# Optimization experiments

Hardware: AMD Instinct MI355X
Metric: run time of the kernel (lower is better)

## Reference

```python
import jax, jax.numpy as jnp
from jax import lax
import numpy as np

EPS = 1e-5
ALPHA = 0.2  # LeakyReLU slope


def setup_inputs() -> dict:
    key = jax.random.key(0)
    ks = jax.random.split(key, 8)
    B, N, F_IN, HID, OUT, H = 32, 512, 256, 512, 512, 4
    D = OUT // H
    return {
        "x": jax.random.normal(ks[0], (B, N, F_IN), dtype=jnp.float32),
        "adj": jax.random.uniform(ks[1], (N, N), dtype=jnp.float32),
        "gc_w": jax.random.normal(ks[2], (F_IN, HID), dtype=jnp.float32) * 0.04,
        "gc_b": jax.random.normal(ks[3], (HID,), dtype=jnp.float32) * 0.04,
        "bn1_g": jnp.ones((HID,), jnp.float32),
        "bn1_b": jnp.zeros((HID,), jnp.float32),
        "bn1_m": jnp.zeros((HID,), jnp.float32),
        "bn1_v": jnp.ones((HID,), jnp.float32),
        "gat_w": jax.random.normal(ks[4], (H, D, HID), dtype=jnp.float32) * 0.04,
        "conv_w": jax.random.normal(ks[5], (OUT, OUT, 3), dtype=jnp.float32) * 0.02,
        "conv_b": jax.random.normal(ks[6], (OUT,), dtype=jnp.float32) * 0.02,
        "bn2_g": jnp.ones((OUT,), jnp.float32),
        "bn2_b": jnp.zeros((OUT,), jnp.float32),
        "bn2_m": jnp.zeros((OUT,), jnp.float32),
        "bn2_v": jnp.ones((OUT,), jnp.float32),
    }


def reference(x, adj, gc_w, gc_b, bn1_g, bn1_b, bn1_m, bn1_v, gat_w,
              conv_w, conv_b, bn2_g, bn2_b, bn2_m, bn2_v):
    # --- GraphConvolution: adj @ (x @ W) + b ---
    support = jnp.einsum('bnc,cd->bnd', x, gc_w)
    g = jnp.einsum('nm,bmd->bnd', adj, support) + gc_b  # [B,N,HID]
    # --- BatchNorm1d over channel dim (eval mode) + ReLU ---
    g = (g - bn1_m) * (bn1_g / jnp.sqrt(bn1_v + EPS)) + bn1_b
    g = jax.nn.relu(g)
    # --- Multi-head GAT (repeat/mul/sum == attention-weighted matmul) ---
    hh = jnp.einsum('bnf,hdf->bhnd', g, gat_w)           # per-head projections
    e = jnp.einsum('bhnd,bhmd->bhnm', hh, hh)            # logits [B,H,N,N]
    e = jnp.where(e > 0, e, ALPHA * e)                   # LeakyReLU
    att = jax.nn.softmax(e, axis=-1)
    o = jnp.einsum('bhnm,bhmd->bhnd', att, hh)
    B, H, N, D = o.shape
    o = o.transpose(0, 2, 1, 3).reshape(B, N, H * D)     # concat heads [B,N,OUT]
    # --- TCN block: conv1d(k=3,pad=1) over node axis + BN(eval) + ReLU ---
    xc = o.transpose(0, 2, 1)                            # [B,C,N]
    y = lax.conv_general_dilated(xc, conv_w, (1,), ((1, 1),),
                                 dimension_numbers=('NCH', 'OIH', 'NCH'))
    y = y + conv_b[None, :, None]
    y = (y - bn2_m[None, :, None]) * (bn2_g / jnp.sqrt(bn2_v + EPS))[None, :, None] + bn2_b[None, :, None]
    y = jax.nn.relu(y)
    return y.transpose(0, 2, 1)                          # [B,N,OUT]
```

## Files before the change

kernel.cpp:

```cpp
#include <hip/hip_runtime.h>
#include <math.h>

#define BATCH 32
#define NNODE 512
#define FIN   256
#define HIDC  512
#define OUTC  512
#define NHEAD 4
#define HDIM  128
#define EPSV  1e-5f
#define ALPHA_LR 0.2f

typedef _Float16 half8 __attribute__((ext_vector_type(8)));
typedef _Float16 half4v __attribute__((ext_vector_type(4)));
typedef float floatx4 __attribute__((ext_vector_type(4)));

#define GLOBAL_TO_LDS16(g, l)                                                  \
  __builtin_amdgcn_global_load_lds(                                            \
      (const __attribute__((address_space(1))) void*)(g),                      \
      (__attribute__((address_space(3))) void*)(l), 16, 0, 0)

__device__ __forceinline__ void split_gemm_acc(
    const _Float16* __restrict__ Ah, const _Float16* __restrict__ Al, int lda,
    const _Float16* __restrict__ Bh, const _Float16* __restrict__ Bl, int ldb,
    int K, int rowBase, int colBase,
    _Float16* sAh, _Float16* sAl, _Float16* sBh, _Float16* sBl,
    floatx4 acc[4][4], int tid) {
  const int lane = tid & 63, wave = tid >> 6;
  const int wr = (wave >> 1) * 64, wc = (wave & 1) * 64;
  const int fr = lane & 15, q = lane >> 4;
  const int r = tid >> 2;
  const int cks = (((tid & 3) ^ ((r >> 1) & 3))) * 8;
  const int qx = (q ^ ((fr >> 1) & 3)) * 8;
  for (int k0 = 0; k0 < K; k0 += 32) {
    GLOBAL_TO_LDS16(&Ah[(size_t)(rowBase + r) * lda + k0 + cks], &sAh[tid * 8]);
    GLOBAL_TO_LDS16(&Ah[(size_t)(rowBase + r + 64) * lda + k0 + cks], &sAh[2048 + tid * 8]);
    GLOBAL_TO_LDS16(&Al[(size_t)(rowBase + r) * lda + k0 + cks], &sAl[tid * 8]);
    GLOBAL_TO_LDS16(&Al[(size_t)(rowBase + r + 64) * lda + k0 + cks], &sAl[2048 + tid * 8]);
    GLOBAL_TO_LDS16(&Bh[(size_t)(colBase + r) * ldb + k0 + cks], &sBh[tid * 8]);
    GLOBAL_TO_LDS16(&Bh[(size_t)(colBase + r + 64) * ldb + k0 + cks], &sBh[2048 + tid * 8]);
    GLOBAL_TO_LDS16(&Bl[(size_t)(colBase + r) * ldb + k0 + cks], &sBl[tid * 8]);
    GLOBAL_TO_LDS16(&Bl[(size_t)(colBase + r + 64) * ldb + k0 + cks], &sBl[2048 + tid * 8]);
    __syncthreads();
    half8 ah[4], al4[4], bh[4], bl4[4];
#pragma unroll
    for (int i = 0; i < 4; ++i) {
      ah[i]  = *(const half8*)&sAh[(wr + i * 16 + fr) * 32 + qx];
      al4[i] = *(const half8*)&sAl[(wr + i * 16 + fr) * 32 + qx];
    }
#pragma unroll
    for (int j = 0; j < 4; ++j) {
      bh[j]  = *(const half8*)&sBh[(wc + j * 16 + fr) * 32 + qx];
      bl4[j] = *(const half8*)&sBl[(wc + j * 16 + fr) * 32 + qx];
    }
#pragma unroll
    for (int i = 0; i < 4; ++i)
#pragma unroll
      for (int j = 0; j < 4; ++j) {
        acc[i][j] = __builtin_amdgcn_mfma_f32_16x16x32_f16(al4[i], bh[j], acc[i][j], 0, 0, 0);
        acc[i][j] = __builtin_amdgcn_mfma_f32_16x16x32_f16(ah[i], bl4[j], acc[i][j], 0, 0, 0);
        acc[i][j] = __builtin_amdgcn_mfma_f32_16x16x32_f16(ah[i], bh[j], acc[i][j], 0, 0, 0);
      }
    __syncthreads();
  }
}

__global__ __launch_bounds__(256) void k_prep(
    const float* __restrict__ adj, const float* __restrict__ gcw,
    const float* __restrict__ gatw, const float* __restrict__ cw,
    _Float16* __restrict__ ADJh, _Float16* __restrict__ ADJl,
    _Float16* __restrict__ GWh, _Float16* __restrict__ GWl,
    _Float16* __restrict__ GAh, _Float16* __restrict__ GAl,
    _Float16* __restrict__ WT, _Float16* __restrict__ OP) {
  const int i = blockIdx.x * 256 + threadIdx.x;
  if (i < 262144) {
    float v = adj[i];
    _Float16 h = (_Float16)v;
    ADJh[i] = h; ADJl[i] = (_Float16)(v - (float)h);
  } else if (i < 393216) {
    int j = i - 262144;
    int n = j >> 8, k = j & 255;
    float v = gcw[(size_t)k * HIDC + n];
    _Float16 h = (_Float16)v;
    GWh[j] = h; GWl[j] = (_Float16)(v - (float)h);
  } else if (i < 655360) {
    int j = i - 393216;
    float v = gatw[j];
    _Float16 h = (_Float16)v;
    GAh[j] = h; GAl[j] = (_Float16)(v - (float)h);
  } else if (i < 1441792) {
    int j = i - 655360;
    int n = j / 1536, kk = j - n * 1536;
    int tap = kk >> 9, ci = kk & 511;
    WT[j] = (_Float16)cw[(size_t)n * 1536 + ci * 3 + tap];
  } else if (i < 1474560) {
    int j = i - 1441792;
    int b = j >> 10, rs = (j >> 9) & 1, c = j & 511;
    OP[((size_t)b * 514 + rs * 513) * OUTC + c] = (_Float16)0.f;
  }
}

__global__ __launch_bounds__(256) void k_xsplit(const float* __restrict__ X,
                                                _Float16* __restrict__ Xh,
                                                _Float16* __restrict__ Xl) {
  const int i = (blockIdx.x * 256 + threadIdx.x) * 4;
  float4 v = *(const float4*)&X[i];
  half4v h, l;
  h[0] = (_Float16)v.x; l[0] = (_Float16)(v.x - (float)h[0]);
  h[1] = (_Float16)v.y; l[1] = (_Float16)(v.y - (float)h[1]);
  h[2] = (_Float16)v.z; l[2] = (_Float16)(v.z - (float)h[2]);
  h[3] = (_Float16)v.w; l[3] = (_Float16)(v.w - (float)h[3]);
  *(half4v*)&Xh[i] = h;
  *(half4v*)&Xl[i] = l;
}

__global__ __launch_bounds__(256) void k_support_t(
    const _Float16* __restrict__ GWh, const _Float16* __restrict__ GWl,
    const _Float16* __restrict__ Xh, const _Float16* __restrict__ Xl,
    _Float16* __restrict__ STh, _Float16* __restrict__ STl) {
  __shared__ _Float16 sm[4][4096];
  const int tid = threadIdx.x;
  const int rowBase = blockIdx.y * 128, colBase = blockIdx.x * 128;
  floatx4 acc[4][4] = {};
  split_gemm_acc(GWh, GWl, FIN, Xh, Xl, FIN, FIN, rowBase, colBase,
                 sm[0], sm[1], sm[2], sm[3], acc, tid);
  const int lane = tid & 63, wave = tid >> 6;
  const int wr = (wave >> 1) * 64, wc = (wave & 1) * 64;
  const int fr = lane & 15, q = lane >> 4;
#pragma unroll
  for (int i = 0; i < 4; ++i) {
    const int ch0 = rowBase + wr + i * 16 + q * 4;
#pragma unroll
    for (int rg = 0; rg < 4; ++rg) {
      size_t base = (size_t)(ch0 + rg) * 16384 + colBase + wc + fr;
#pragma unroll
      for (int j = 0; j < 4; ++j) {
        float v = acc[i][j][rg];
        _Float16 h = (_Float16)v;
        STh[base + j * 16] = h;
        STl[base + j * 16] = (_Float16)(v - (float)h);
      }
    }
  }
}

__global__ __launch_bounds__(256) void k_gcn(
    const _Float16* __restrict__ ADJh, const _Float16* __restrict__ ADJl,
    const _Float16* __restrict__ STh, const _Float16* __restrict__ STl,
    const float* __restrict__ gcb, const float* __restrict__ g1,
    const float* __restrict__ b1, const float* __restrict__ m1,
    const float* __restrict__ v1,
    _Float16* __restrict__ Gh, _Float16* __restrict__ Gl) {
  __shared__ _Float16 sm[4][4096];
  const int tid = threadIdx.x;
  const int rowBase = blockIdx.y * 128, colBase = blockIdx.x * 128;
  const int b = blockIdx.z;
  floatx4 acc[4][4] = {};
  split_gemm_acc(ADJh, ADJl, NNODE, STh + (size_t)b * NNODE, STl + (size_t)b * NNODE,
                 16384, NNODE, rowBase, colBase, sm[0], sm[1], sm[2], sm[3], acc, tid);
  const int lane = tid & 63, wave = tid >> 6;
  const int wr = (wave >> 1) * 64, wc = (wave & 1) * 64;
  const int fr = lane & 15, q = lane >> 4;
  float sc[4], of[4];
#pragma unroll
  for (int j = 0; j < 4; ++j) {
    int c = colBase + wc + j * 16 + fr;
    float s = g1[c] * rsqrtf(v1[c] + EPSV);
    sc[j] = s;
    of[j] = (gcb[c] - m1[c]) * s + b1[c];
  }
#pragma unroll
  for (int i = 0; i < 4; ++i) {
    const int n0 = rowBase + wr + i * 16 + q * 4;
#pragma unroll
    for (int rg = 0; rg < 4; ++rg) {
      size_t base = ((size_t)b * NNODE + n0 + rg) * HIDC + colBase + wc + fr;
#pragma unroll
      for (int j = 0; j < 4; ++j) {
        float v = fmaxf(fmaf(acc[i][j][rg], sc[j], of[j]), 0.0f);
        _Float16 h = (_Float16)v;
        Gh[base + j * 16] = h;
        Gl[base + j * 16] = (_Float16)(v - (float)h);
      }
    }
  }
}

__global__ __launch_bounds__(256) void k_hh(
    const _Float16* __restrict__ Gh, const _Float16* __restrict__ Gl,
    const _Float16* __restrict__ GAh, const _Float16* __restrict__ GAl,
    _Float16* __restrict__ HHh, _Float16* __restrict__ HHl) {
  __shared__ _Float16 sm[4][4096];
  const int tid = threadIdx.x;
  const int rowBase = blockIdx.y * 128, colBase = blockIdx.x * 128;
  floatx4 acc[4][4] = {};
  split_gemm_acc(Gh, Gl, HIDC, GAh, GAl, HIDC, HIDC, rowBase, colBase,
                 sm[0], sm[1], sm[2], sm[3], acc, tid);
  const int lane = tid & 63, wave = tid >> 6;
  const int wr = (wave >> 1) * 64, wc = (wave & 1) * 64;
  const int fr = lane & 15, q = lane >> 4;
#pragma unroll
  for (int i = 0; i < 4; ++i) {
    const int r0 = rowBase + wr + i * 16 + q * 4;
#pragma unroll
    for (int rg = 0; rg < 4; ++rg) {
      size_t base = (size_t)(r0 + rg) * OUTC + colBase + wc + fr;
#pragma unroll
      for (int j = 0; j < 4; ++j) {
        float v = acc[i][j][rg];
        _Float16 h = (_Float16)v;
        HHh[base + j * 16] = h;
        HHl[base + j * 16] = (_Float16)(v - (float)h);
      }
    }
  }
}

__global__ __launch_bounds__(256) void k_vt(const _Float16* __restrict__ HHh,
                                            _Float16* __restrict__ HHT) {
  __shared__ _Float16 sT[128 * 132];
  const int bt = blockIdx.x;
  const int nt = bt & 3, g = bt >> 2;
  const int bb = g >> 2, h = g & 3;
  const int tid = threadIdx.x;
  const int rr = tid >> 4, cc = (tid & 15) * 8;
#pragma unroll
  for (int it = 0; it < 8; ++it) {
    int node = rr + it * 16;
    half8 v = *(const half8*)&HHh[((size_t)bb * 512 + nt * 128 + node) * 512 + h * 128 + cc];
#pragma unroll
    for (int e = 0; e < 8; ++e) sT[(cc + e) * 132 + node] = v[e];
  }
  __syncthreads();
#pragma unroll
  for (int it = 0; it < 8; ++it) {
    int d = rr + it * 16;
    half8 v;
#pragma unroll
    for (int e = 0; e < 8; ++e) v[e] = sT[d * 132 + cc + e];
    *(half8*)&HHT[((size_t)g * 128 + d) * 512 + nt * 128 + cc] = v;
  }
}

__global__ __launch_bounds__(256, 3) void k_attn(
    const _Float16* __restrict__ HHh, const _Float16* __restrict__ HHl,
    const _Float16* __restrict__ HHT, _Float16* __restrict__ OP) {
  __shared__ _Float16 sK[8][2048];
  __shared__ _Float16 sP[64 * 68];
  _Float16* sV = &sK[0][0];
  const int tid = threadIdx.x;
  const int lane = tid & 63, wave = tid >> 6;
  const int fr = lane & 15, q = lane >> 4;
  const int id = blockIdx.x;
  const int slot = id >> 3;
  const int g = (id & 7) + 8 * (slot >> 3);
  const int qBase = (slot & 7) * 64;
  const int bb = g >> 2, h = g & 3;
  const int w16 = wave * 16;
  const _Float16* Qh = HHh + (size_t)bb * NNODE * OUTC + h * HDIM;
  const _Float16* Ql = HHl + (size_t)bb * NNODE * OUTC + h * HDIM;
  const _Float16* VT = HHT + (size_t)g * HDIM * NNODE;
  const int rk = tid >> 2;
  const int cks = (((tid & 3) ^ ((rk >> 1) & 3))) * 8;
  const int qx = (q ^ ((fr >> 1) & 3)) * 8;

  half8 qh[4], ql[4];
#pragma unroll
  for (int k0 = 0; k0 < 4; ++k0) {
    const size_t off = (size_t)(qBase + w16 + fr) * OUTC + k0 * 32 + q * 8;
    qh[k0] = *(const half8*)&Qh[off];
    ql[k0] = *(const half8*)&Ql[off];
  }

  floatx4 oacc[8] = {};
  float m_i[4], l_i[4];
#pragma unroll
  for (int rg = 0; rg < 4; ++rg) { m_i[rg] = -1e30f; l_i[rg] = 0.f; }

  for (int kt = 0; kt < 8; ++kt) {
    const int ktb = kt * 64;
#pragma unroll
    for (int t = 0; t < 4; ++t) {
      GLOBAL_TO_LDS16(&Qh[(size_t)(ktb + rk) * OUTC + t * 32 + cks], &sK[t][tid * 8]);
      GLOBAL_TO_LDS16(&Ql[(size_t)(ktb + rk) * OUTC + t * 32 + cks], &sK[4 + t][tid * 8]);
    }
    __syncthreads();
    floatx4 sacc[4] = {};
#pragma unroll
    for (int k0 = 0; k0 < 4; ++k0)
#pragma unroll
      for (int j = 0; j < 4; ++j) {
        half8 bh = *(const half8*)&sK[k0][(j * 16 + fr) * 32 + qx];
        half8 bl = *(const half8*)&sK[4 + k0][(j * 16 + fr) * 32 + qx];
        sacc[j] = __builtin_amdgcn_mfma_f32_16x16x32_f16(ql[k0], bh, sacc[j], 0, 0, 0);
        sacc[j] = __builtin_amdgcn_mfma_f32_16x16x32_f16(qh[k0], bl, sacc[j], 0, 0, 0);
        sacc[j] = __builtin_amdgcn_mfma_f32_16x16x32_f16(qh[k0], bh, sacc[j], 0, 0, 0);
      }
    __syncthreads();
#pragma unroll
    for (int j = 0; j < 4; ++j)
#pragma unroll
      for (int rg = 0; rg < 4; ++rg) {
        float v = sacc[j][rg];
        sacc[j][rg] = v > 0.f ? v : ALPHA_LR * v;
      }
#pragma unroll
    for (int rg = 0; rg < 4; ++rg) {
      float mx = sacc[0][rg];
#pragma unroll
      for (int j = 1; j < 4; ++j) mx = fmaxf(mx, sacc[j][rg]);
      mx = fmaxf(mx, __shfl_xor(mx, 1));
      mx = fmaxf(mx, __shfl_xor(mx, 2));
      mx = fmaxf(mx, __shfl_xor(mx, 4));
      mx = fmaxf(mx, __shfl_xor(mx, 8));
      float mnew = fmaxf(m_i[rg], mx);
      float alpha = __expf(m_i[rg] - mnew);
      m_i[rg] = mnew;
      float sum = 0.f;
#pragma unroll
      for (int j = 0; j < 4; ++j) {
        float p = __expf(sacc[j][rg] - mnew);
        sacc[j][rg] = p;
        sum += p;
      }
      sum += __shfl_xor(sum, 1);
      sum += __shfl_xor(sum, 2);
      sum += __shfl_xor(sum, 4);
      sum += __shfl_xor(sum, 8);
      l_i[rg] = l_i[rg] * alpha + sum;
#pragma unroll
      for (int j = 0; j < 8; ++j) oacc[j][rg] *= alpha;
    }
#pragma unroll
    for (int l = 0; l < 4; ++l)
      GLOBAL_TO_LDS16(&VT[(size_t)((l >> 1) * 64 + rk) * NNODE + ktb + (l & 1) * 32 + cks],
                      &sV[(l & 1) * 4096 + (l >> 1) * 2048 + tid * 8]);
#pragma unroll
    for (int j = 0; j < 4; ++j)
#pragma unroll
      for (int rg = 0; rg < 4; ++rg)
        sP[(w16 + q * 4 + rg) * 68 + j * 16 + fr] = (_Float16)sacc[j][rg];
    __syncthreads();
#pragma unroll
    for (int ks = 0; ks < 2; ++ks) {
      half8 pa = *(const half8*)&sP[(w16 + fr) * 68 + ks * 32 + q * 8];
#pragma unroll
      for (int j = 0; j < 8; ++j) {
        half8 bv = *(const half8*)&sV[ks * 4096 + (j * 16 + fr) * 32 + qx];
        oacc[j] = __builtin_amdgcn_mfma_f32_16x16x32_f16(pa, bv, oacc[j], 0, 0, 0);
      }
    }
    __syncthreads();
  }
#pragma unroll
  for (int rg = 0; rg < 4; ++rg) {
    const float inv = 1.0f / l_i[rg];
    const int node = qBase + w16 + q * 4 + rg;
    size_t base = ((size_t)bb * 514 + 1 + node) * OUTC + h * HDIM + fr;
#pragma unroll
    for (int j = 0; j < 8; ++j)
      OP[base + j * 16] = (_Float16)(oacc[j][rg] * inv);
  }
}

__global__ __launch_bounds__(256) void k_conv_mfma(
    const _Float16* __restrict__ OP, const _Float16* __restrict__ WT,
    const float* __restrict__ cb, const float* __restrict__ g2,
    const float* __restrict__ b2, const float* __restrict__ m2,
    const float* __restrict__ v2, float* __restrict__ Y) {
  __shared__ _Float16 At[128 * 32];
  __shared__ _Float16 Bt[128 * 32];
  const int tid = threadIdx.x;
  const int lane = tid & 63, wave = tid >> 6;
  const int wr = (wave >> 1) * 64, wc = (wave & 1) * 64;
  const int id = blockIdx.y * 4 + blockIdx.x;
  const int jj = id >> 3;
  const int rowBase = ((id & 7) * 16 + (jj >> 2)) * 128;
  const int colBase = (jj & 3) * 128;
  const int b = rowBase >> 9;
  const int n0 = rowBase & 511;
  const int r = tid >> 2;
  const int cks = (((tid & 3) ^ ((r >> 1) & 3))) * 8;
  const int fr = lane & 15, q = lane >> 4;
  const int qx = (q ^ ((fr >> 1) & 3)) * 8;
  floatx4 acc[4][4] = {};
  for (int k0 = 0; k0 < 3 * OUTC; k0 += 32) {
    const int tap = k0 >> 9;
    const int cib = k0 & 511;
    const size_t abase = ((size_t)b * 514 + n0 + tap) * OUTC + cib + cks;
    GLOBAL_TO_LDS16(&OP[abase + (size_t)r * OUTC],        &At[tid * 8]);
    GLOBAL_TO_LDS16(&OP[abase + (size_t)(r + 64) * OUTC], &At[2048 + tid * 8]);
    GLOBAL_TO_LDS16(&WT[(size_t)(colBase + r) * 1536 + k0 + cks],      &Bt[tid * 8]);
    GLOBAL_TO_LDS16(&WT[(size_t)(colBase + r + 64) * 1536 + k0 + cks], &Bt[2048 + tid * 8]);
    __syncthreads();
    half8 af[4], bf[4];
#pragma unroll
    for (int i = 0; i < 4; ++i)
      af[i] = *(const half8*)&At[(wr + i * 16 + fr) * 32 + qx];
#pragma unroll
    for (int j = 0; j < 4; ++j)
      bf[j] = *(const half8*)&Bt[(wc + j * 16 + fr) * 32 + qx];
#pragma unroll
    for (int i = 0; i < 4; ++i)
#pragma unroll
      for (int j = 0; j < 4; ++j)
        acc[i][j] = __builtin_amdgcn_mfma_f32_16x16x32_f16(af[i], bf[j], acc[i][j], 0, 0, 0);
    __syncthreads();
  }
  float sc[4], of[4];
#pragma unroll
  for (int j = 0; j < 4; ++j) {
    int c = colBase + wc + j * 16 + fr;
    float s = g2[c] * rsqrtf(v2[c] + EPSV);
    sc[j] = s;
    of[j] = (cb[c] - m2[c]) * s + b2[c];
  }
#pragma unroll
  for (int i = 0; i < 4; ++i) {
    const int R0r = rowBase + wr + i * 16 + q * 4;
#pragma unroll
    for (int rg = 0; rg < 4; ++rg) {
      float* dst = &Y[(size_t)(R0r + rg) * OUTC + colBase + wc + fr];
#pragma unroll
      for (int j = 0; j < 4; ++j)
        dst[j * 16] = fmaxf(fmaf(acc[i][j][rg], sc[j], of[j]), 0.0f);
    }
  }
}

extern "C" void kernel_launch(void* const* d_in, const int* in_sizes, int n_in,
                              void* d_out, int out_size, void* d_ws, size_t ws_size,
                              hipStream_t stream) {
  const float* x     = (const float*)d_in[0];
  const float* adj   = (const float*)d_in[1];
  const float* gc_w  = (const float*)d_in[2];
  const float* gc_b  = (const float*)d_in[3];
  const float* bn1_g = (const float*)d_in[4];
  const float* bn1_b = (const float*)d_in[5];
  const float* bn1_m = (const float*)d_in[6];
  const float* bn1_v = (const float*)d_in[7];
  const float* gat_w = (const float*)d_in[8];
  const float* conv_w= (const float*)d_in[9];
  const float* conv_b= (const float*)d_in[10];
  const float* bn2_g = (const float*)d_in[11];
  const float* bn2_b = (const float*)d_in[12];
  const float* bn2_m = (const float*)d_in[13];
  const float* bn2_v = (const float*)d_in[14];
  float* out = (float*)d_out;

  char* ws = (char*)d_ws;
  _Float16* STh = (_Float16*)(ws + 0);
  _Float16* STl = (_Float16*)(ws + 16777216);
  _Float16* HHh = (_Float16*)(ws + 0);
  _Float16* HHl = (_Float16*)(ws + 16777216);
  _Float16* Xh  = (_Float16*)(ws + 33554432);
  _Float16* Xl  = (_Float16*)(ws + 41943040);
  _Float16* Gh  = (_Float16*)(ws + 33554432);
  _Float16* Gl  = (_Float16*)(ws + 50331648);
  _Float16* HHT = (_Float16*)(ws + 33554432);
  _Float16* OP  = (_Float16*)(ws + 67108864);
  _Float16* WT  = (_Float16*)(ws + 83951616);
  _Float16* ADJh= (_Float16*)(ws + 85524480);
  _Float16* ADJl= (_Float16*)(ws + 86048768);
  _Float16* GWh = (_Float16*)(ws + 86573056);
  _Float16* GWl = (_Float16*)(ws + 86835200);
  _Float16* GAh = (_Float16*)(ws + 87097344);
  _Float16* GAl = (_Float16*)(ws + 87621632);

  k_prep<<<5760, 256, 0, stream>>>(adj, gc_w, gat_w, conv_w,
                                   ADJh, ADJl, GWh, GWl, GAh, GAl, WT, OP);
  k_xsplit<<<4096, 256, 0, stream>>>(x, Xh, Xl);
  k_support_t<<<dim3(128, 4), 256, 0, stream>>>(GWh, GWl, Xh, Xl, STh, STl);
  k_gcn<<<dim3(4, 4, 32), 256, 0, stream>>>(ADJh, ADJl, STh, STl, gc_b,
                                            bn1_g, bn1_b, bn1_m, bn1_v, Gh, Gl);
  k_hh<<<dim3(4, 128), 256, 0, stream>>>(Gh, Gl, GAh, GAl, HHh, HHl);
  k_vt<<<512, 256, 0, stream>>>(HHh, HHT);
  k_attn<<<1024, 256, 0, stream>>>(HHh, HHl, HHT, OP);
  k_conv_mfma<<<dim3(4, 128), 256, 0, stream>>>(OP, WT, conv_b,
                                                bn2_g, bn2_b, bn2_m, bn2_v, out);
}
```

Before: 290.0 us.

## Double-buffer LDS tiles in split GEMM and conv MFMA loops

```diff
diff --git a/kernel.cpp b/kernel.cpp
--- a/kernel.cpp
+++ b/kernel.cpp
@@ -32,26 +32,36 @@
   const int r = tid >> 2;
   const int cks = (((tid & 3) ^ ((r >> 1) & 3))) * 8;
   const int qx = (q ^ ((fr >> 1) & 3)) * 8;
+
+  auto stage = [&](int buf, int k0) {
+    const int o = buf * 4096;
+    GLOBAL_TO_LDS16(&Ah[(size_t)(rowBase + r) * lda + k0 + cks], &sAh[o + tid * 8]);
+    GLOBAL_TO_LDS16(&Ah[(size_t)(rowBase + r + 64) * lda + k0 + cks], &sAh[o + 2048 + tid * 8]);
+    GLOBAL_TO_LDS16(&Al[(size_t)(rowBase + r) * lda + k0 + cks], &sAl[o + tid * 8]);
+    GLOBAL_TO_LDS16(&Al[(size_t)(rowBase + r + 64) * lda + k0 + cks], &sAl[o + 2048 + tid * 8]);
+    GLOBAL_TO_LDS16(&Bh[(size_t)(colBase + r) * ldb + k0 + cks], &sBh[o + tid * 8]);
+    GLOBAL_TO_LDS16(&Bh[(size_t)(colBase + r + 64) * ldb + k0 + cks], &sBh[o + 2048 + tid * 8]);
+    GLOBAL_TO_LDS16(&Bl[(size_t)(colBase + r) * ldb + k0 + cks], &sBl[o + tid * 8]);
+    GLOBAL_TO_LDS16(&Bl[(size_t)(colBase + r + 64) * ldb + k0 + cks], &sBl[o + 2048 + tid * 8]);
+  };
+
+  stage(0, 0);
+  __syncthreads();
+  int cur = 0;
   for (int k0 = 0; k0 < K; k0 += 32) {
-    GLOBAL_TO_LDS16(&Ah[(size_t)(rowBase + r) * lda + k0 + cks], &sAh[tid * 8]);
-    GLOBAL_TO_LDS16(&Ah[(size_t)(rowBase + r + 64) * lda + k0 + cks], &sAh[2048 + tid * 8]);
-    GLOBAL_TO_LDS16(&Al[(size_t)(rowBase + r) * lda + k0 + cks], &sAl[tid * 8]);
-    GLOBAL_TO_LDS16(&Al[(size_t)(rowBase + r + 64) * lda + k0 + cks], &sAl[2048 + tid * 8]);
-    GLOBAL_TO_LDS16(&Bh[(size_t)(colBase + r) * ldb + k0 + cks], &sBh[tid * 8]);
-    GLOBAL_TO_LDS16(&Bh[(size_t)(colBase + r + 64) * ldb + k0 + cks], &sBh[2048 + tid * 8]);
-    GLOBAL_TO_LDS16(&Bl[(size_t)(colBase + r) * ldb + k0 + cks], &sBl[tid * 8]);
-    GLOBAL_TO_LDS16(&Bl[(size_t)(colBase + r + 64) * ldb + k0 + cks], &sBl[2048 + tid * 8]);
-    __syncthreads();
+    const bool more = (k0 + 32 < K);
+    if (more) stage(cur ^ 1, k0 + 32);
+    const int o = cur * 4096;
     half8 ah[4], al4[4], bh[4], bl4[4];
 #pragma unroll
     for (int i = 0; i < 4; ++i) {
-      ah[i]  = *(const half8*)&sAh[(wr + i * 16 + fr) * 32 + qx];
-      al4[i] = *(const half8*)&sAl[(wr + i * 16 + fr) * 32 + qx];
+      ah[i]  = *(const half8*)&sAh[o + (wr + i * 16 + fr) * 32 + qx];
+      al4[i] = *(const half8*)&sAl[o + (wr + i * 16 + fr) * 32 + qx];
     }
 #pragma unroll
     for (int j = 0; j < 4; ++j) {
-      bh[j]  = *(const half8*)&sBh[(wc + j * 16 + fr) * 32 + qx];
-      bl4[j] = *(const half8*)&sBl[(wc + j * 16 + fr) * 32 + qx];
+      bh[j]  = *(const half8*)&sBh[o + (wc + j * 16 + fr) * 32 + qx];
+      bl4[j] = *(const half8*)&sBl[o + (wc + j * 16 + fr) * 32 + qx];
     }
 #pragma unroll
     for (int i = 0; i < 4; ++i)
@@ -61,7 +71,10 @@
         acc[i][j] = __builtin_amdgcn_mfma_f32_16x16x32_f16(ah[i], bl4[j], acc[i][j], 0, 0, 0);
         acc[i][j] = __builtin_amdgcn_mfma_f32_16x16x32_f16(ah[i], bh[j], acc[i][j], 0, 0, 0);
       }
-    __syncthreads();
+    if (more) {
+      __syncthreads();
+      cur ^= 1;
+    }
   }
 }
 
@@ -118,7 +131,7 @@
     const _Float16* __restrict__ GWh, const _Float16* __restrict__ GWl,
     const _Float16* __restrict__ Xh, const _Float16* __restrict__ Xl,
     _Float16* __restrict__ STh, _Float16* __restrict__ STl) {
-  __shared__ _Float16 sm[4][4096];
+  __shared__ _Float16 sm[4][8192];
   const int tid = threadIdx.x;
   const int rowBase = blockIdx.y * 128, colBase = blockIdx.x * 128;
   floatx4 acc[4][4] = {};
@@ -151,7 +164,7 @@
     const float* __restrict__ b1, const float* __restrict__ m1,
     const float* __restrict__ v1,
     _Float16* __restrict__ Gh, _Float16* __restrict__ Gl) {
-  __shared__ _Float16 sm[4][4096];
+  __shared__ _Float16 sm[4][8192];
   const int tid = threadIdx.x;
   const int rowBase = blockIdx.y * 128, colBase = blockIdx.x * 128;
   const int b = blockIdx.z;
@@ -190,7 +203,7 @@
     const _Float16* __restrict__ Gh, const _Float16* __restrict__ Gl,
     const _Float16* __restrict__ GAh, const _Float16* __restrict__ GAl,
     _Float16* __restrict__ HHh, _Float16* __restrict__ HHl) {
-  __shared__ _Float16 sm[4][4096];
+  __shared__ _Float16 sm[4][8192];
   const int tid = threadIdx.x;
   const int rowBase = blockIdx.y * 128, colBase = blockIdx.x * 128;
   floatx4 acc[4][4] = {};
@@ -368,8 +381,8 @@
     const float* __restrict__ cb, const float* __restrict__ g2,
     const float* __restrict__ b2, const float* __restrict__ m2,
     const float* __restrict__ v2, float* __restrict__ Y) {
-  __shared__ _Float16 At[128 * 32];
-  __shared__ _Float16 Bt[128 * 32];
+  __shared__ _Float16 At[2][4096];
+  __shared__ _Float16 Bt[2][4096];
   const int tid = threadIdx.x;
   const int lane = tid & 63, wave = tid >> 6;
   const int wr = (wave >> 1) * 64, wc = (wave & 1) * 64;
@@ -383,29 +396,40 @@
   const int cks = (((tid & 3) ^ ((r >> 1) & 3))) * 8;
   const int fr = lane & 15, q = lane >> 4;
   const int qx = (q ^ ((fr >> 1) & 3)) * 8;
-  floatx4 acc[4][4] = {};
-  for (int k0 = 0; k0 < 3 * OUTC; k0 += 32) {
+
+  auto stage = [&](int buf, int k0) {
     const int tap = k0 >> 9;
     const int cib = k0 & 511;
     const size_t abase = ((size_t)b * 514 + n0 + tap) * OUTC + cib + cks;
-    GLOBAL_TO_LDS16(&OP[abase + (size_t)r * OUTC],        &At[tid * 8]);
-    GLOBAL_TO_LDS16(&OP[abase + (size_t)(r + 64) * OUTC], &At[2048 + tid * 8]);
-    GLOBAL_TO_LDS16(&WT[(size_t)(colBase + r) * 1536 + k0 + cks],      &Bt[tid * 8]);
-    GLOBAL_TO_LDS16(&WT[(size_t)(colBase + r + 64) * 1536 + k0 + cks], &Bt[2048 + tid * 8]);
-    __syncthreads();
+    GLOBAL_TO_LDS16(&OP[abase + (size_t)r * OUTC],        &At[buf][tid * 8]);
+    GLOBAL_TO_LDS16(&OP[abase + (size_t)(r + 64) * OUTC], &At[buf][2048 + tid * 8]);
+    GLOBAL_TO_LDS16(&WT[(size_t)(colBase + r) * 1536 + k0 + cks],      &Bt[buf][tid * 8]);
+    GLOBAL_TO_LDS16(&WT[(size_t)(colBase + r + 64) * 1536 + k0 + cks], &Bt[buf][2048 + tid * 8]);
+  };
+
+  floatx4 acc[4][4] = {};
+  stage(0, 0);
+  __syncthreads();
+  int cur = 0;
+  for (int k0 = 0; k0 < 3 * OUTC; k0 += 32) {
+    const bool more = (k0 + 32 < 3 * OUTC);
+    if (more) stage(cur ^ 1, k0 + 32);
     half8 af[4], bf[4];
 #pragma unroll
     for (int i = 0; i < 4; ++i)
-      af[i] = *(const half8*)&At[(wr + i * 16 + fr) * 32 + qx];
+      af[i] = *(const half8*)&At[cur][(wr + i * 16 + fr) * 32 + qx];
 #pragma unroll
     for (int j = 0; j < 4; ++j)
-      bf[j] = *(const half8*)&Bt[(wc + j * 16 + fr) * 32 + qx];
+      bf[j] = *(const half8*)&Bt[cur][(wc + j * 16 + fr) * 32 + qx];
 #pragma unroll
     for (int i = 0; i < 4; ++i)
 #pragma unroll
       for (int j = 0; j < 4; ++j)
         acc[i][j] = __builtin_amdgcn_mfma_f32_16x16x32_f16(af[i], bf[j], acc[i][j], 0, 0, 0);
-    __syncthreads();
+    if (more) {
+      __syncthreads();
+      cur ^= 1;
+    }
   }
   float sc[4], of[4];
 #pragma unroll
```

Measured after the change: 301.3 us. +3.9%, slower.

## Process two query sub-tiles per wave in attention to double K/V reuse

Applied to the files above, without the earlier changes.

```diff
diff --git a/kernel.cpp b/kernel.cpp
--- a/kernel.cpp
+++ b/kernel.cpp
@@ -242,21 +242,21 @@
   }
 }
 
-__global__ __launch_bounds__(256, 3) void k_attn(
+__global__ __launch_bounds__(256, 2) void k_attn(
     const _Float16* __restrict__ HHh, const _Float16* __restrict__ HHl,
     const _Float16* __restrict__ HHT, _Float16* __restrict__ OP) {
   __shared__ _Float16 sK[8][2048];
-  __shared__ _Float16 sP[64 * 68];
+  __shared__ _Float16 sP[128 * 68];
   _Float16* sV = &sK[0][0];
   const int tid = threadIdx.x;
   const int lane = tid & 63, wave = tid >> 6;
   const int fr = lane & 15, q = lane >> 4;
   const int id = blockIdx.x;
   const int slot = id >> 3;
-  const int g = (id & 7) + 8 * (slot >> 3);
-  const int qBase = (slot & 7) * 64;
+  const int g = (id & 7) + 8 * (slot >> 2);
+  const int qBase = (slot & 3) * 128;
   const int bb = g >> 2, h = g & 3;
-  const int w16 = wave * 16;
+  const int w32 = wave * 32;
   const _Float16* Qh = HHh + (size_t)bb * NNODE * OUTC + h * HDIM;
   const _Float16* Ql = HHl + (size_t)bb * NNODE * OUTC + h * HDIM;
   const _Float16* VT = HHT + (size_t)g * HDIM * NNODE;
@@ -264,18 +264,22 @@
   const int cks = (((tid & 3) ^ ((rk >> 1) & 3))) * 8;
   const int qx = (q ^ ((fr >> 1) & 3)) * 8;
 
-  half8 qh[4], ql[4];
-#pragma unroll
-  for (int k0 = 0; k0 < 4; ++k0) {
-    const size_t off = (size_t)(qBase + w16 + fr) * OUTC + k0 * 32 + q * 8;
-    qh[k0] = *(const half8*)&Qh[off];
-    ql[k0] = *(const half8*)&Ql[off];
-  }
-
-  floatx4 oacc[8] = {};
-  float m_i[4], l_i[4];
-#pragma unroll
-  for (int rg = 0; rg < 4; ++rg) { m_i[rg] = -1e30f; l_i[rg] = 0.f; }
+  half8 qh[2][4], ql[2][4];
+#pragma unroll
+  for (int m = 0; m < 2; ++m)
+#pragma unroll
+    for (int k0 = 0; k0 < 4; ++k0) {
+      const size_t off = (size_t)(qBase + w32 + m * 16 + fr) * OUTC + k0 * 32 + q * 8;
+      qh[m][k0] = *(const half8*)&Qh[off];
+      ql[m][k0] = *(const half8*)&Ql[off];
+    }
+
+  floatx4 oacc[2][8] = {};
+  float m_i[2][4], l_i[2][4];
+#pragma unroll
+  for (int m = 0; m < 2; ++m)
+#pragma unroll
+    for (int rg = 0; rg < 4; ++rg) { m_i[m][rg] = -1e30f; l_i[m][rg] = 0.f; }
 
   for (int kt = 0; kt < 8; ++kt) {
     const int ktb = kt * 64;
@@ -285,82 +289,94 @@
       GLOBAL_TO_LDS16(&Ql[(size_t)(ktb + rk) * OUTC + t * 32 + cks], &sK[4 + t][tid * 8]);
     }
     __syncthreads();
-    floatx4 sacc[4] = {};
+    floatx4 sacc[2][4] = {};
 #pragma unroll
     for (int k0 = 0; k0 < 4; ++k0)
 #pragma unroll
       for (int j = 0; j < 4; ++j) {
         half8 bh = *(const half8*)&sK[k0][(j * 16 + fr) * 32 + qx];
         half8 bl = *(const half8*)&sK[4 + k0][(j * 16 + fr) * 32 + qx];
-        sacc[j] = __builtin_amdgcn_mfma_f32_16x16x32_f16(ql[k0], bh, sacc[j], 0, 0, 0);
-        sacc[j] = __builtin_amdgcn_mfma_f32_16x16x32_f16(qh[k0], bl, sacc[j], 0, 0, 0);
-        sacc[j] = __builtin_amdgcn_mfma_f32_16x16x32_f16(qh[k0], bh, sacc[j], 0, 0, 0);
-      }
-    __syncthreads();
-#pragma unroll
-    for (int j = 0; j < 4; ++j)
+#pragma unroll
+        for (int m = 0; m < 2; ++m) {
+          sacc[m][j] = __builtin_amdgcn_mfma_f32_16x16x32_f16(ql[m][k0], bh, sacc[m][j], 0, 0, 0);
+          sacc[m][j] = __builtin_amdgcn_mfma_f32_16x16x32_f16(qh[m][k0], bl, sacc[m][j], 0, 0, 0);
+          sacc[m][j] = __builtin_amdgcn_mfma_f32_16x16x32_f16(qh[m][k0], bh, sacc[m][j], 0, 0, 0);
+        }
+      }
+    __syncthreads();
+#pragma unroll
+    for (int m = 0; m < 2; ++m) {
+#pragma unroll
+      for (int j = 0; j < 4; ++j)
+#pragma unroll
+        for (int rg = 0; rg < 4; ++rg) {
+          float v = sacc[m][j][rg];
+          sacc[m][j][rg] = v > 0.f ? v : ALPHA_LR * v;
+        }
 #pragma unroll
       for (int rg = 0; rg < 4; ++rg) {
-        float v = sacc[j][rg];
-        sacc[j][rg] = v > 0.f ? v : ALPHA_LR * v;
-      }
-#pragma unroll
-    for (int rg = 0; rg < 4; ++rg) {
-      float mx = sacc[0][rg];
-#pragma unroll
-      for (int j = 1; j < 4; ++j) mx = fmaxf(mx, sacc[j][rg]);
-      mx = fmaxf(mx, __shfl_xor(mx, 1));
-      mx = fmaxf(mx, __shfl_xor(mx, 2));
-      mx = fmaxf(mx, __shfl_xor(mx, 4));
-      mx = fmaxf(mx, __shfl_xor(mx, 8));
-      float mnew = fmaxf(m_i[rg], mx);
-      float alpha = __expf(m_i[rg] - mnew);
-      m_i[rg] = mnew;
-      float sum = 0.f;
-#pragma unroll
-      for (int j = 0; j < 4; ++j) {
-        float p = __expf(sacc[j][rg] - mnew);
-        sacc[j][rg] = p;
-        sum += p;
-      }
-      sum += __shfl_xor(sum, 1);
-      sum += __shfl_xor(sum, 2);
-      sum += __shfl_xor(sum, 4);
-      sum += __shfl_xor(sum, 8);
-      l_i[rg] = l_i[rg] * alpha + sum;
-#pragma unroll
-      for (int j = 0; j < 8; ++j) oacc[j][rg] *= alpha;
+        float mx = sacc[m][0][rg];
+#pragma unroll
+        for (int j = 1; j < 4; ++j) mx = fmaxf(mx, sacc[m][j][rg]);
+        mx = fmaxf(mx, __shfl_xor(mx, 1));
+        mx = fmaxf(mx, __shfl_xor(mx, 2));
+        mx = fmaxf(mx, __shfl_xor(mx, 4));
+        mx = fmaxf(mx, __shfl_xor(mx, 8));
+        float mnew = fmaxf(m_i[m][rg], mx);
+        float alpha = __expf(m_i[m][rg] - mnew);
+        m_i[m][rg] = mnew;
+        float sum = 0.f;
+#pragma unroll
+        for (int j = 0; j < 4; ++j) {
+          float p = __expf(sacc[m][j][rg] - mnew);
+          sacc[m][j][rg] = p;
+          sum += p;
+        }
+        sum += __shfl_xor(sum, 1);
+        sum += __shfl_xor(sum, 2);
+        sum += __shfl_xor(sum, 4);
+        sum += __shfl_xor(sum, 8);
+        l_i[m][rg] = l_i[m][rg] * alpha + sum;
+#pragma unroll
+        for (int j = 0; j < 8; ++j) oacc[m][j][rg] *= alpha;
+      }
     }
 #pragma unroll
     for (int l = 0; l < 4; ++l)
       GLOBAL_TO_LDS16(&VT[(size_t)((l >> 1) * 64 + rk) * NNODE + ktb + (l & 1) * 32 + cks],
                       &sV[(l & 1) * 4096 + (l >> 1) * 2048 + tid * 8]);
 #pragma unroll
-    for (int j = 0; j < 4; ++j)
-#pragma unroll
-      for (int rg = 0; rg < 4; ++rg)
-        sP[(w16 + q * 4 + rg) * 68 + j * 16 + fr] = (_Float16)sacc[j][rg];
+    for (int m = 0; m < 2; ++m)
+#pragma unroll
+      for (int j = 0; j < 4; ++j)
+#pragma unroll
+        for (int rg = 0; rg < 4; ++rg)
+          sP[(w32 + m * 16 + q * 4 + rg) * 68 + j * 16 + fr] = (_Float16)sacc[m][j][rg];
     __syncthreads();
 #pragma unroll
     for (int ks = 0; ks < 2; ++ks) {
-      half8 pa = *(const half8*)&sP[(w16 + fr) * 68 + ks * 32 + q * 8];
+      half8 pa0 = *(const half8*)&sP[(w32 + fr) * 68 + ks * 32 + q * 8];
+      half8 pa1 = *(const half8*)&sP[(w32 + 16 + fr) * 68 + ks * 32 + q * 8];
 #pragma unroll
       for (int j = 0; j < 8; ++j) {
         half8 bv = *(const half8*)&sV[ks * 4096 + (j * 16 + fr) * 32 + qx];
-        oacc[j] = __builtin_amdgcn_mfma_f32_16x16x32_f16(pa, bv, oacc[j], 0, 0, 0);
-      }
-    }
-    __syncthreads();
-  }
-#pragma unroll
-  for (int rg = 0; rg < 4; ++rg) {
-    const float inv = 1.0f / l_i[rg];
-    const int node = qBase + w16 + q * 4 + rg;
-    size_t base = ((size_t)bb * 514 + 1 + node) * OUTC + h * HDIM + fr;
-#pragma unroll
-    for (int j = 0; j < 8; ++j)
-      OP[base + j * 16] = (_Float16)(oacc[j][rg] * inv);
-  }
+        oacc[0][j] = __builtin_amdgcn_mfma_f32_16x16x32_f16(pa0, bv, oacc[0][j], 0, 0, 0);
+        oacc[1][j] = __builtin_amdgcn_mfma_f32_16x16x32_f16(pa1, bv, oacc[1][j], 0, 0, 0);
+      }
+    }
+    __syncthreads();
+  }
+#pragma unroll
+  for (int m = 0; m < 2; ++m)
+#pragma unroll
+    for (int rg = 0; rg < 4; ++rg) {
+      const float inv = 1.0f / l_i[m][rg];
+      const int node = qBase + w32 + m * 16 + q * 4 + rg;
+      size_t base = ((size_t)bb * 514 + 1 + node) * OUTC + h * HDIM + fr;
+#pragma unroll
+      for (int j = 0; j < 8; ++j)
+        OP[base + j * 16] = (_Float16)(oacc[m][j][rg] * inv);
+    }
 }
 
 __global__ __launch_bounds__(256) void k_conv_mfma(
@@ -475,7 +491,7 @@
                                             bn1_g, bn1_b, bn1_m, bn1_v, Gh, Gl);
   k_hh<<<dim3(4, 128), 256, 0, stream>>>(Gh, Gl, GAh, GAl, HHh, HHl);
   k_vt<<<512, 256, 0, stream>>>(HHh, HHT);
-  k_attn<<<1024, 256, 0, stream>>>(HHh, HHl, HHT, OP);
+  k_attn<<<512, 256, 0, stream>>>(HHh, HHl, HHT, OP);
   k_conv_mfma<<<dim3(4, 128), 256, 0, stream>>>(OP, WT, conv_b,
                                                 bn2_g, bn2_b, bn2_m, bn2_v, out);
 }
```

Result: faster. 278.1 us (-4.1%).
